# Kernel optimization log

Hardware: AMD Instinct MI355X
Metric: run time of the kernel (lower is better)

The kernel has to match this reference:

```python
import jax, jax.numpy as jnp
import numpy as np


def setup_inputs() -> dict:
    key = jax.random.key(0)
    ks = jax.random.split(key, 8)
    B, S, H = 16, 512, 1024
    K, E, L = 32, 1024, 2  # max_node_length, max_edge_length=K**2, num_labels
    seq = jax.random.normal(ks[0], (B, S, H), jnp.float32)
    # structured cumulative proof offsets: col0=1 ('<s>' offset, skipped by forward),
    # then n increasing offsets, zeros terminate. n <= K-1 so NAF node fits in K slots.
    rng = np.random.default_rng(0)
    off = np.zeros((B, K), np.int64)
    off[:, 0] = 1
    for b in range(B):
        n = int(rng.integers(8, K))  # 8..31 segment nodes
        lens = rng.integers(4, 14, size=n)
        off[b, 1:n + 1] = np.cumsum(lens)  # max < 31*13+1 < S
    s = 0.02
    w = lambda k, shp: jax.random.normal(k, shp, jnp.float32) * s
    return {
        'sequence_outputs': seq,
        'proof_offsets': jnp.asarray(off),
        'naf_W': w(ks[1], (H, H)), 'naf_b': jnp.zeros((H,), jnp.float32),
        'cls_dense_W': w(ks[2], (H, H)), 'cls_dense_b': jnp.zeros((H,), jnp.float32),
        'cls_out_W': w(ks[3], (H, L)), 'cls_out_b': jnp.zeros((L,), jnp.float32),
        'node_dense_W': w(ks[4], (H, H)), 'node_dense_b': jnp.zeros((H,), jnp.float32),
        'node_out_W': w(ks[5], (H, L)), 'node_out_b': jnp.zeros((L,), jnp.float32),
        'edge_dense_W': w(ks[6], (3 * H, H)), 'edge_dense_b': jnp.zeros((H,), jnp.float32),
        'edge_out_W': w(ks[7], (H, L)), 'edge_out_b': jnp.zeros((L,), jnp.float32),
        'max_node_length': K,
        'max_edge_length': E,
    }


def _head(x, dW, db, oW, ob):
    # dropout is identity in eval mode
    return jnp.tanh(x @ dW + db) @ oW + ob


def reference(sequence_outputs, proof_offsets,
              naf_W, naf_b, cls_dense_W, cls_dense_b, cls_out_W, cls_out_b,
              node_dense_W, node_dense_b, node_out_W, node_out_b,
              edge_dense_W, edge_dense_b, edge_out_W, edge_out_b,
              max_node_length, max_edge_length):
    B, S, H = sequence_outputs.shape
    K = max_node_length
    E = max_edge_length
    cls_tok = sequence_outputs[:, 0, :]                      # [B,H]
    naf = cls_tok @ naf_W + naf_b                            # [B,H]
    logits = _head(cls_tok, cls_dense_W, cls_dense_b, cls_out_W, cls_out_b)  # [B,L]

    # segment-mean pooling over variable-length spans
    off = proof_offsets[:, 1:]                               # [B,K-1] cumulative offsets
    valid = off > 0                                          # [B,K-1]
    n = valid.sum(axis=1)                                    # [B] #segment nodes
    starts = jnp.concatenate([jnp.ones((B, 1), off.dtype), off[:, :-1] + 1], axis=1)
    pos = jnp.arange(S)
    mask = ((pos[None, None, :] >= starts[:, :, None])
            & (pos[None, None, :] <= off[:, :, None])
            & valid[:, :, None]).astype(sequence_outputs.dtype)  # [B,K-1,S]
    sums = jnp.einsum('bks,bsh->bkh', mask, sequence_outputs)
    counts = mask.sum(axis=-1, keepdims=True)
    node_emb = sums / jnp.maximum(counts, 1.0)               # [B,K-1,H]

    # place segment nodes in slots [0,n), NAF at slot n, zeros after (padded batch buffer)
    slots = jnp.arange(K)
    is_naf = slots[None, :] == n[:, None]
    is_node = slots[None, :] < n[:, None]
    node_emb_p = jnp.pad(node_emb, ((0, 0), (0, 1), (0, 0)))  # [B,K,H]
    full_nodes = jnp.where(is_naf[:, :, None], naf[:, None, :],
                           jnp.where(is_node[:, :, None], node_emb_p, 0.0))  # [B,K,H]

    node_logits = _head(full_nodes, node_dense_W, node_dense_b, node_out_W, node_out_b)

    # pairwise edge features, row-major flattened per sample with m=n+1 nodes:
    # edge[i*m+j] = [node[j], node[i], node[j]-node[i]]
    m = n + 1                                                # [B]
    e = jnp.arange(E)
    i_idx = e[None, :] // m[:, None]                         # [B,E]
    j_idx = e[None, :] % m[:, None]
    valid_e = e[None, :] < (m * m)[:, None]
    i_c = jnp.clip(i_idx, 0, K - 1)
    j_c = jnp.clip(j_idx, 0, K - 1)
    ni = jnp.take_along_axis(full_nodes, i_c[:, :, None], axis=1)  # [B,E,H]
    nj = jnp.take_along_axis(full_nodes, j_c[:, :, None], axis=1)
    edge_feat = jnp.where(valid_e[:, :, None],
                          jnp.concatenate([nj, ni, nj - ni], axis=-1), 0.0)  # [B,E,3H]

    edge_logits = _head(edge_feat, edge_dense_W, edge_dense_b, edge_out_W, edge_out_b)

    return logits, node_logits, edge_logits
```

## Files before the change

### kernel.cpp

```cpp
#include <hip/hip_runtime.h>
#include <hip/hip_bf16.h>

typedef __hip_bfloat16 bf16;
typedef unsigned short ushort;
typedef __attribute__((ext_vector_type(8))) short short8v;
typedef __attribute__((ext_vector_type(4))) float float4v;

__device__ __forceinline__ float us2f(unsigned int u) {
    union { unsigned int i; float f; } c; c.i = u << 16; return c.f;
}
__device__ __forceinline__ bf16 f2bf(float x) { return __float2bfloat16(x); }
__device__ __forceinline__ ushort f2bfu(float x) {
    union { float f; unsigned int i; } c; c.f = x;
    unsigned int lsb = (c.i >> 16) & 1;
    return (ushort)((c.i + 0x7FFF + lsb) >> 16);
}
__device__ __forceinline__ float fcf(float x) {
    return fminf(1000.f, fmaxf(-1000.f, x));
}
__device__ __forceinline__ int iclamp(int v, int lo, int hi) {
    return v < lo ? lo : (v > hi ? hi : v);
}

__device__ __forceinline__ int po_ps(const int* po) {
    return ((po[1] | po[3] | po[5]) == 0) ? 2 : 1;
}
__device__ __forceinline__ int count_n(const int* po, int b, int ps) {
    int n = 0;
    #pragma unroll
    for (int j = 1; j < 32; ++j) n += (po[(b * 32 + j) * ps] > 0) ? 1 : 0;
    return iclamp(n, 0, 31);
}

__global__ __launch_bounds__(256) void k_sentinel(float* __restrict__ out, int nv, float val) {
    int i = blockIdx.x * 256 + threadIdx.x;
    if (i < nv) out[i] = val;
}


__device__ __forceinline__ void dev_prep(int kt, int nt, int z, int tid,
                                         const float* __restrict__ ndW,
                                         const float* __restrict__ eW,
                                         ushort* __restrict__ Wct, float* smemf)
{
    float (*T)[33] = (float (*)[33])smemf;

    const int k_loc = tid >> 3, n0 = (tid & 7) * 4;
    const size_t gofs = (size_t)(kt * 32 + k_loc) * 1024 + nt * 32 + n0;
    float4 v;
    if (z == 0) {
        v = *(const float4*)(ndW + gofs);
    } else if (z == 1) {
        float4 a = *(const float4*)(eW + gofs);
        float4 b = *(const float4*)(eW + (size_t)2048 * 1024 + gofs);
        v = make_float4(a.x + b.x, a.y + b.y, a.z + b.z, a.w + b.w);
    } else {
        float4 a = *(const float4*)(eW + (size_t)1024 * 1024 + gofs);
        float4 b = *(const float4*)(eW + (size_t)2048 * 1024 + gofs);
        v = make_float4(a.x - b.x, a.y - b.y, a.z - b.z, a.w - b.w);
    }
    T[k_loc][n0 + 0] = v.x; T[k_loc][n0 + 1] = v.y;
    T[k_loc][n0 + 2] = v.z; T[k_loc][n0 + 3] = v.w;
    __syncthreads();

    const int n_loc = tid >> 3, k0 = (tid & 7) * 4;
    ushort* dst = Wct + (size_t)z * 1024 * 1024 + (size_t)(nt * 32 + n_loc) * 1024 + kt * 32 + k0;
    ushort4 o;
    o.x = f2bfu(T[k0 + 0][n_loc]); o.y = f2bfu(T[k0 + 1][n_loc]);
    o.z = f2bfu(T[k0 + 2][n_loc]); o.w = f2bfu(T[k0 + 3][n_loc]);
    *(ushort4*)dst = o;
}

__device__ __forceinline__ void dev_nodes(int bx, int tid,
                                          const float* __restrict__ seq,
                                          const int* __restrict__ po,
                                          bf16* __restrict__ fn, int bbase)
{
    const int b_loc = bx >> 5;
    const int k = bx & 31;
    const int b = bbase + b_loc;
    const int ps = po_ps(po);
    const int n = count_n(po, b, ps);
    if (k == n) return;

    const int h0 = tid * 4;
    float4 acc = make_float4(0.f, 0.f, 0.f, 0.f);
    if (k < n) {
        int s_end   = iclamp(po[(b * 32 + k + 1) * ps], 1, 511);
        int s_begin = (k == 0) ? 1 : iclamp(po[(b * 32 + k) * ps] + 1, 1, 511);
        if (s_end < s_begin) s_end = s_begin;
        const float inv = 1.0f / (float)(s_end - s_begin + 1);
        for (int s = s_begin; s <= s_end; ++s) {
            float4 u = *(const float4*)(seq + ((size_t)(b * 512 + s)) * 1024 + h0);
            acc.x += u.x; acc.y += u.y; acc.z += u.z; acc.w += u.w;
        }
        acc.x *= inv; acc.y *= inv; acc.z *= inv; acc.w *= inv;
    }
    bf16* dst = fn + (size_t)(b_loc * 32 + k) * 1024 + h0;
    dst[0] = f2bf(acc.x); dst[1] = f2bf(acc.y); dst[2] = f2bf(acc.z); dst[3] = f2bf(acc.w);
}

__device__ __forceinline__ void dev_cls(int b_loc, int q, int tid,
                                        const float* __restrict__ seq,
                                        const int* __restrict__ po,
                                        const float* __restrict__ nafW, const float* __restrict__ nafb,
                                        const float* __restrict__ clsW, const float* __restrict__ clsb,
                                        const float* __restrict__ clsoW,
                                        bf16* __restrict__ fn,
                                        float* __restrict__ cacc,
                                        int bbase, float* smemf)
{
    const int b = bbase + b_loc;
    const int c = tid & 63, kq = tid >> 6;
    const int hout = q * 64 + c;
    float* xs  = smemf;
    float* red = smemf + 1024;
    for (int j = tid; j < 1024; j += 256) xs[j] = seq[(size_t)b * 524288 + j];
    __syncthreads();

    float ca = 0.f, na = 0.f;
    const int kb = kq * 256;
    for (int i = 0; i < 256; ++i) {
        const int k = kb + i;
        float x = xs[k];
        ca = fmaf(x, clsW[(size_t)k * 1024 + hout], ca);
        na = fmaf(x, nafW[(size_t)k * 1024 + hout], na);
    }
    red[kq * 64 + c] = ca; red[(4 + kq) * 64 + c] = na;
    __syncthreads();
    if (kq == 0) {
        ca = red[0 * 64 + c] + red[1 * 64 + c] + red[2 * 64 + c] + red[3 * 64 + c];
        na = red[4 * 64 + c] + red[5 * 64 + c] + red[6 * 64 + c] + red[7 * 64 + c];
        const int ps = po_ps(po);
        const int n = count_n(po, b, ps);
        fn[(size_t)(b_loc * 32 + n) * 1024 + hout] = f2bf(na + nafb[hout]);
        float h = tanhf(ca + clsb[hout]);
        float2 ow = ((const float2*)clsoW)[hout];
        float q0 = h * ow.x, q1 = h * ow.y;
        #pragma unroll
        for (int off = 32; off > 0; off >>= 1) {
            q0 += __shfl_down(q0, off, 64);
            q1 += __shfl_down(q1, off, 64);
        }
        if (c == 0) {
            cacc[(b_loc * 16 + q) * 2 + 0] = q0;
            cacc[(b_loc * 16 + q) * 2 + 1] = q1;
        }
    }
}

__device__ __forceinline__ void dev_econ(int tid,
                                         const float* __restrict__ edb,
                                         const float* __restrict__ eoW,
                                         float* __restrict__ econ)
{
    if (tid >= 64) return;
    const int lane = tid;
    float a0 = 0.f, a1 = 0.f;
    #pragma unroll
    for (int c = 0; c < 16; ++c) {
        const int idx = c * 64 + lane;
        float t = tanhf(edb[idx]);
        float2 ow = ((const float2*)eoW)[idx];
        a0 = fmaf(t, ow.x, a0);
        a1 = fmaf(t, ow.y, a1);
    }
    #pragma unroll
    for (int off = 32; off > 0; off >>= 1) {
        a0 += __shfl_down(a0, off, 64);
        a1 += __shfl_down(a1, off, 64);
    }
    if (lane == 0) { econ[0] = a0; econ[1] = a1; }
}

__global__ __launch_bounds__(256) void k_fusedA(const float* __restrict__ seq,
                                                const int* __restrict__ po,
                                                const float* __restrict__ nafW, const float* __restrict__ nafb,
                                                const float* __restrict__ clsW, const float* __restrict__ clsb,
                                                const float* __restrict__ clsoW,
                                                const float* __restrict__ ndW,
                                                const float* __restrict__ eW,
                                                const float* __restrict__ edb,
                                                const float* __restrict__ eoW,
                                                bf16* __restrict__ fn,
                                                float* __restrict__ cacc,
                                                ushort* __restrict__ Wct,
                                                float* __restrict__ econ)
{
    __shared__ float smem[1536];
    const int blk = blockIdx.x;
    const int tid = threadIdx.x;
    if (blk < 3072) {
        const int z = blk >> 10, rem = blk & 1023;
        dev_prep(rem & 31, rem >> 5, z, tid, ndW, eW, Wct, smem);
    } else if (blk < 3584) {
        dev_nodes(blk - 3072, tid, seq, po, fn, 0);
    } else if (blk < 3840) {
        const int r = blk - 3584;
        dev_cls(r & 15, r >> 4, tid, seq, po, nafW, nafb, clsW, clsb, clsoW, fn, cacc, 0, smem);
    } else {
        dev_econ(tid, edb, eoW, econ);
    }
}

__global__ __launch_bounds__(256) void k_nodes(const float* __restrict__ seq,
                                               const int* __restrict__ po,
                                               bf16* __restrict__ fn, int bbase)
{
    dev_nodes(blockIdx.x, threadIdx.x, seq, po, fn, bbase);
}
__global__ __launch_bounds__(256) void k_cls(const float* __restrict__ seq,
                                             const int* __restrict__ po,
                                             const float* __restrict__ nafW, const float* __restrict__ nafb,
                                             const float* __restrict__ clsW, const float* __restrict__ clsb,
                                             const float* __restrict__ clsoW,
                                             bf16* __restrict__ fn,
                                             float* __restrict__ cacc, int bbase)
{
    __shared__ float smem[1536];
    dev_cls(blockIdx.x, blockIdx.y, threadIdx.x, seq, po, nafW, nafb, clsW, clsb, clsoW, fn, cacc, bbase, smem);
}

__global__ __launch_bounds__(256) void k_huv_mfma(const bf16* __restrict__ X,
                                                  const ushort* __restrict__ Wct,
                                                  const float* __restrict__ ndb,
                                                  const float* __restrict__ noW,
                                                  float* __restrict__ nacc,
                                                  bf16* __restrict__ U,
                                                  bf16* __restrict__ V)
{
    const int rt = blockIdx.x;
    const int cc = blockIdx.y;
    const int z  = blockIdx.z;
    const int tid = threadIdx.x;
    const int w = tid >> 6, lane = tid & 63;
    const int quad = lane >> 4, l16 = lane & 15;
    const int rbase = rt * 16;

    __shared__ char smem[32768];
    short* A_lds = (short*)smem;
    float* Rs    = (float*)smem;

    {
        const int r = tid >> 4, s = tid & 15;
        const ushort* src = (const ushort*)X + (size_t)(rbase + r) * 1024 + s * 64;
        #pragma unroll
        for (int cch = 0; cch < 8; ++cch) {
            const int k0 = s * 64 + cch * 8;
            uint4 v = *(const uint4*)(src + cch * 8);
            const int slot = ((k0 >> 5) * 64 + ((k0 >> 3) & 3) * 16 + r) * 8;
            *(uint4*)&A_lds[slot] = v;
        }
    }
    __syncthreads();

    const ushort* Wz = Wct + (size_t)z * 1024 * 1024;
    const int nbase = cc * 128 + w * 32;
    const ushort* B0 = Wz + (size_t)(nbase + l16) * 1024 + quad * 8;
    const ushort* B1 = B0 + (size_t)16 * 1024;

    float4v acc0 = {0.f, 0.f, 0.f, 0.f};
    float4v acc1 = {0.f, 0.f, 0.f, 0.f};

    #pragma unroll 4
    for (int ks = 0; ks < 1024; ks += 32) {
        short8v a  = *(const short8v*)&A_lds[((ks >> 5) * 64 + quad * 16 + l16) * 8];
        short8v b0 = *(const short8v*)(B0 + ks);
        short8v b1 = *(const short8v*)(B1 + ks);
        acc0 = __builtin_amdgcn_mfma_f32_16x16x32_bf16(a, b0, acc0, 0, 0, 0);
        acc1 = __builtin_amdgcn_mfma_f32_16x16x32_bf16(a, b1, acc1, 0, 0, 0);
    }
    __syncthreads();

    #pragma unroll
    for (int reg = 0; reg < 4; ++reg) {
        Rs[(quad * 4 + reg) * 128 + w * 32 + l16]      = acc0[reg];
        Rs[(quad * 4 + reg) * 128 + w * 32 + 16 + l16] = acc1[reg];
    }
    __syncthreads();

    const int row = tid >> 4;
    const int c0 = (tid & 15) * 8;
    const int gcol0 = cc * 128 + c0;
    const float* src = &Rs[row * 128 + c0];
    float s[8];
    {
        float4 a = ((const float4*)src)[0];
        float4 b = ((const float4*)src)[1];
        s[0] = a.x; s[1] = a.y; s[2] = a.z; s[3] = a.w;
        s[4] = b.x; s[5] = b.y; s[6] = b.z; s[7] = b.w;
    }
    if (z == 0) {
        float q0 = 0.f, q1 = 0.f;
        #pragma unroll
        for (int e = 0; e < 8; ++e) {
            float t = tanhf(s[e] + ndb[gcol0 + e]);
            float2 ow = ((const float2*)noW)[gcol0 + e];
            q0 = fmaf(t, ow.x, q0);
            q1 = fmaf(t, ow.y, q1);
        }
        #pragma unroll
        for (int off = 8; off > 0; off >>= 1) {
            q0 += __shfl_down(q0, off, 16);
            q1 += __shfl_down(q1, off, 16);
        }
        if ((tid & 15) == 0) {
            float* np = nacc + ((size_t)(rbase + row) * 8 + cc) * 2;
            np[0] = q0; np[1] = q1;
        }
    } else {
        bf16* dstbuf = (z == 1) ? U : V;
        bf16* dst = dstbuf + (size_t)(rbase + row) * 1024 + gcol0;
        #pragma unroll
        for (int e = 0; e < 8; ++e) dst[e] = f2bf(s[e]);
    }
}

__global__ __launch_bounds__(256) void k_huv_valu(const bf16* __restrict__ X,
                                                  const float* __restrict__ ndW, const float* __restrict__ ndb,
                                                  const float* __restrict__ noW,
                                                  const float* __restrict__ eW,
                                                  float* __restrict__ nacc,
                                                  bf16* __restrict__ U,
                                                  bf16* __restrict__ V)
{
    const int rt = blockIdx.x, cc = blockIdx.y, z = blockIdx.z;
    const int tid = threadIdx.x;
    const int w = tid >> 6, lane = tid & 63;
    const int rg = lane >> 4, cg = lane & 15;
    const int rbase = rt * 16;
    const int colb = cc * 128 + cg * 8;

    __shared__ float LDSb[8192];
    float* Xs = LDSb;
    float* Rs = LDSb;

    const float* W0;
    const float* W1 = nullptr;
    float sgn = 1.f;
    if (z == 0)      { W0 = ndW; }
    else if (z == 1) { W0 = eW; W1 = eW + (size_t)2048 * 1024; }
    else             { W0 = eW + (size_t)1024 * 1024; W1 = eW + (size_t)2048 * 1024; sgn = -1.f; }

    float acc[32];
    #pragma unroll
    for (int i = 0; i < 32; ++i) acc[i] = 0.f;

    const int sr = tid & 15, sq0 = tid >> 4;
    const ushort* Xu = (const ushort*)X;

    for (int ks = 0; ks < 1024; ks += 256) {
        __syncthreads();
        #pragma unroll
        for (int it = 0; it < 4; ++it) {
            int qq = sq0 + it * 16;
            ushort4 xv = *(const ushort4*)(Xu + (size_t)(rbase + sr) * 1024 + ks + qq * 4);
            int kk = qq * 4;
            Xs[(kk + 0) * 16 + sr] = us2f(xv.x);
            Xs[(kk + 1) * 16 + sr] = us2f(xv.y);
            Xs[(kk + 2) * 16 + sr] = us2f(xv.z);
            Xs[(kk + 3) * 16 + sr] = us2f(xv.w);
        }
        __syncthreads();
        const int k0 = ks + w * 64;
        for (int kk = 0; kk < 64; ++kk) {
            float4 xv = *(const float4*)&Xs[(w * 64 + kk) * 16 + rg * 4];
            const float* wp0 = W0 + (size_t)(k0 + kk) * 1024 + colb;
            float4 wa = ((const float4*)wp0)[0];
            float4 wb = ((const float4*)wp0)[1];
            if (W1) {
                const float* wp1 = W1 + (size_t)(k0 + kk) * 1024 + colb;
                float4 va = ((const float4*)wp1)[0];
                float4 vb = ((const float4*)wp1)[1];
                wa.x = fmaf(sgn, va.x, wa.x); wa.y = fmaf(sgn, va.y, wa.y);
                wa.z = fmaf(sgn, va.z, wa.z); wa.w = fmaf(sgn, va.w, wa.w);
                wb.x = fmaf(sgn, vb.x, wb.x); wb.y = fmaf(sgn, vb.y, wb.y);
                wb.z = fmaf(sgn, vb.z, wb.z); wb.w = fmaf(sgn, vb.w, wb.w);
            }
            float xr[4] = {xv.x, xv.y, xv.z, xv.w};
            #pragma unroll
            for (int rr = 0; rr < 4; ++rr) {
                acc[rr*8+0] = fmaf(xr[rr], wa.x, acc[rr*8+0]);
                acc[rr*8+1] = fmaf(xr[rr], wa.y, acc[rr*8+1]);
                acc[rr*8+2] = fmaf(xr[rr], wa.z, acc[rr*8+2]);
                acc[rr*8+3] = fmaf(xr[rr], wa.w, acc[rr*8+3]);
                acc[rr*8+4] = fmaf(xr[rr], wb.x, acc[rr*8+4]);
                acc[rr*8+5] = fmaf(xr[rr], wb.y, acc[rr*8+5]);
                acc[rr*8+6] = fmaf(xr[rr], wb.z, acc[rr*8+6]);
                acc[rr*8+7] = fmaf(xr[rr], wb.w, acc[rr*8+7]);
            }
        }
    }
    __syncthreads();
    #pragma unroll
    for (int rr = 0; rr < 4; ++rr) {
        float* dst = &Rs[w * 2048 + (rg * 4 + rr) * 128 + cg * 8];
        *(float4*)(dst)     = make_float4(acc[rr*8+0], acc[rr*8+1], acc[rr*8+2], acc[rr*8+3]);
        *(float4*)(dst + 4) = make_float4(acc[rr*8+4], acc[rr*8+5], acc[rr*8+6], acc[rr*8+7]);
    }
    __syncthreads();
    const int row = tid >> 4;
    const int c0 = (tid & 15) * 8;
    float s[8];
    #pragma unroll
    for (int e = 0; e < 8; ++e) s[e] = 0.f;
    #pragma unroll
    for (int ww = 0; ww < 4; ++ww) {
        const float* src = &Rs[ww * 2048 + row * 128 + c0];
        float4 a = ((const float4*)src)[0];
        float4 b = ((const float4*)src)[1];
        s[0] += a.x; s[1] += a.y; s[2] += a.z; s[3] += a.w;
        s[4] += b.x; s[5] += b.y; s[6] += b.z; s[7] += b.w;
    }
    const int gcol0 = cc * 128 + c0;
    if (z == 0) {
        float q0 = 0.f, q1 = 0.f;
        #pragma unroll
        for (int e = 0; e < 8; ++e) {
            float t = tanhf(s[e] + ndb[gcol0 + e]);
            float2 ow = ((const float2*)noW)[gcol0 + e];
            q0 = fmaf(t, ow.x, q0);
            q1 = fmaf(t, ow.y, q1);
        }
        #pragma unroll
        for (int off = 8; off > 0; off >>= 1) {
            q0 += __shfl_down(q0, off, 16);
            q1 += __shfl_down(q1, off, 16);
        }
        if ((tid & 15) == 0) {
            float* np = nacc + ((size_t)(rbase + row) * 8 + cc) * 2;
            np[0] = q0; np[1] = q1;
        }
    } else {
        bf16* dstbuf = (z == 1) ? U : V;
        bf16* dst = dstbuf + (size_t)(rbase + row) * 1024 + gcol0;
        #pragma unroll
        for (int e = 0; e < 8; ++e) dst[e] = f2bf(s[e]);
    }
}

__global__ __launch_bounds__(256) void k_fin2(const float* __restrict__ nacc,
                                              const float* __restrict__ cacc,
                                              const float* __restrict__ nob,
                                              const float* __restrict__ clsob,
                                              float* __restrict__ out,
                                              int bbase, int nb)
{
    const int idx = blockIdx.x * 256 + threadIdx.x;
    const int R = nb * 32;
    if (idx < R) {
        const float4* p = (const float4*)(nacc + (size_t)idx * 16);
        float4 a = p[0], b4 = p[1], c4 = p[2], d4 = p[3];
        float s0 = a.x + a.z + b4.x + b4.z + c4.x + c4.z + d4.x + d4.z;
        float s1 = a.y + a.w + b4.y + b4.w + c4.y + c4.w + d4.y + d4.w;
        out[32 + bbase * 64 + idx * 2 + 0] = fcf(s0 + nob[0]);
        out[32 + bbase * 64 + idx * 2 + 1] = fcf(s1 + nob[1]);
    } else if (idx < R + nb * 2) {
        const int c = idx - R;
        const int b = c >> 1, l = c & 1;
        float s = 0.f;
        for (int q = 0; q < 16; ++q) s += cacc[(b * 16 + q) * 2 + l];
        out[(bbase + b) * 2 + l] = fcf(s + clsob[l]);
    }
}

__global__ __launch_bounds__(256) void k_edge(const bf16* __restrict__ U,
                                              const bf16* __restrict__ V,
                                              const float* __restrict__ edb,
                                              const float* __restrict__ eoW, const float* __restrict__ eob,
                                              const int* __restrict__ po,
                                              float* __restrict__ out,
                                              int bbase)
{
    const int blk = blockIdx.x;
    const int b_loc = blk >> 8;
    const int b = bbase + b_loc;
    const int tid = threadIdx.x;
    const int w = tid >> 6, lane = tid & 63;
    const int e = (blk & 255) * 4 + w;
    const int ps = po_ps(po);
    const int n = count_n(po, b, ps);
    const int m = n + 1;
    const bool valid = e < m * m;
    int i = 0, j = 0;
    if (valid) { i = e / m; j = e - i * m; }
    i = iclamp(i, 0, 31); j = iclamp(j, 0, 31);

    const ushort* urow = (const ushort*)U + (size_t)(b_loc * 32 + j) * 1024;
    const ushort* vrow = (const ushort*)V + (size_t)(b_loc * 32 + i) * 1024;

    float a0 = 0.f, a1 = 0.f;
    #pragma unroll
    for (int c = 0; c < 16; ++c) {
        const int idx = c * 64 + lane;
        float p = edb[idx];
        if (valid) p += us2f(urow[idx]) + us2f(vrow[idx]);
        float t = tanhf(p);
        float2 ow = ((const float2*)eoW)[idx];
        a0 = fmaf(t, ow.x, a0);
        a1 = fmaf(t, ow.y, a1);
    }
    #pragma unroll
    for (int off = 32; off > 0; off >>= 1) {
        a0 += __shfl_down(a0, off, 64);
        a1 += __shfl_down(a1, off, 64);
    }
    if (lane == 0) {
        const size_t o = 32 + 1024 + (size_t)(b * 1024 + e) * 2;
        out[o + 0] = fcf(a0 + eob[0]);
        out[o + 1] = fcf(a1 + eob[1]);
    }
}

__global__ __launch_bounds__(256) void k_fusedC(const bf16* __restrict__ U,
                                                const bf16* __restrict__ V,
                                                const float* __restrict__ nacc,
                                                const float* __restrict__ cacc,
                                                const float* __restrict__ nob,
                                                const float* __restrict__ clsob,
                                                const float* __restrict__ edb,
                                                const float* __restrict__ eoW,
                                                const float* __restrict__ eob,
                                                const float* __restrict__ econ,
                                                const int* __restrict__ po,
                                                float* __restrict__ out)
{
    const int blk = blockIdx.x;
    const int tid = threadIdx.x;

    if (blk >= 4096) {
        const int idx = (blk - 4096) * 256 + tid;
        if (idx < 512) {
            const float4* p = (const float4*)(nacc + (size_t)idx * 16);
            float4 a = p[0], b4 = p[1], c4 = p[2], d4 = p[3];
            float s0 = a.x + a.z + b4.x + b4.z + c4.x + c4.z + d4.x + d4.z;
            float s1 = a.y + a.w + b4.y + b4.w + c4.y + c4.w + d4.y + d4.w;
            out[32 + idx * 2 + 0] = fcf(s0 + nob[0]);
            out[32 + idx * 2 + 1] = fcf(s1 + nob[1]);
        } else if (idx < 544) {
            const int c = idx - 512;
            const int b = c >> 1, l = c & 1;
            float s = 0.f;
            for (int q = 0; q < 16; ++q) s += cacc[(b * 16 + q) * 2 + l];
            out[b * 2 + l] = fcf(s + clsob[l]);
        }
        return;
    }

    const int b = blk >> 8;
    const int w = tid >> 6, lane = tid & 63;
    const int e = (blk & 255) * 4 + w;
    const int ps = po_ps(po);
    const int n = count_n(po, b, ps);
    const int m = n + 1;
    const size_t o = 32 + 1024 + (size_t)(b * 1024 + e) * 2;

    if (e >= m * m) {
        if (lane == 0) {
            out[o + 0] = fcf(econ[0] + eob[0]);
            out[o + 1] = fcf(econ[1] + eob[1]);
        }
        return;
    }

    int i = e / m, j = e - i * m;
    i = iclamp(i, 0, 31); j = iclamp(j, 0, 31);
    const ushort* urow = (const ushort*)U + (size_t)(b * 32 + j) * 1024;
    const ushort* vrow = (const ushort*)V + (size_t)(b * 32 + i) * 1024;

    float a0 = 0.f, a1 = 0.f;
    #pragma unroll
    for (int c = 0; c < 16; ++c) {
        const int idx = c * 64 + lane;
        float p = edb[idx] + us2f(urow[idx]) + us2f(vrow[idx]);
        float t = tanhf(p);
        float2 ow = ((const float2*)eoW)[idx];
        a0 = fmaf(t, ow.x, a0);
        a1 = fmaf(t, ow.y, a1);
    }
    #pragma unroll
    for (int off = 32; off > 0; off >>= 1) {
        a0 += __shfl_down(a0, off, 64);
        a1 += __shfl_down(a1, off, 64);
    }
    if (lane == 0) {
        out[o + 0] = fcf(a0 + eob[0]);
        out[o + 1] = fcf(a1 + eob[1]);
    }
}

extern "C" void kernel_launch(void* const* d_in, const int* in_sizes, int n_in,
                              void* d_out, int out_size, void* d_ws, size_t ws_size,
                              hipStream_t stream) {
    (void)out_size;
    float* out = (float*)d_out;

    bool ok = (n_in >= 16)
        && in_sizes[0] == 8388608 && in_sizes[1] == 512
        && in_sizes[2] == 1048576 && in_sizes[3] == 1024
        && in_sizes[4] == 1048576 && in_sizes[5] == 1024
        && in_sizes[6] == 2048    && in_sizes[7] == 2
        && in_sizes[8] == 1048576 && in_sizes[9] == 1024
        && in_sizes[10] == 2048   && in_sizes[11] == 2
        && in_sizes[12] == 3145728 && in_sizes[13] == 1024
        && in_sizes[14] == 2048   && in_sizes[15] == 2;
    if (!ok) {
        hipLaunchKernelGGL(k_sentinel, dim3(133), dim3(256), 0, stream, out, 33824, 111.0f);
        return;
    }

    const float* seq   = (const float*)d_in[0];
    const int*   po    = (const int*)d_in[1];
    const float* nafW  = (const float*)d_in[2];
    const float* nafb  = (const float*)d_in[3];
    const float* clsW  = (const float*)d_in[4];
    const float* clsb  = (const float*)d_in[5];
    const float* clsoW = (const float*)d_in[6];
    const float* clsob = (const float*)d_in[7];
    const float* ndW   = (const float*)d_in[8];
    const float* ndb   = (const float*)d_in[9];
    const float* noW   = (const float*)d_in[10];
    const float* nob   = (const float*)d_in[11];
    const float* eW    = (const float*)d_in[12];
    const float* edb   = (const float*)d_in[13];
    const float* eoW   = (const float*)d_in[14];
    const float* eob   = (const float*)d_in[15];

    char* ws = (char*)d_ws;

    const size_t fnB   = (size_t)512 * 1024 * 2;
    const size_t naccB = (size_t)512 * 8 * 2 * sizeof(float);
    const size_t caccB = (size_t)16 * 16 * 2 * sizeof(float);
    const size_t econB = 64;
    const size_t wctB  = (size_t)3 * 1024 * 1024 * 2;
    const size_t needA = 3 * fnB + naccB + caccB + econB + wctB;
    const size_t needB = 3 * fnB + naccB + caccB;
    const size_t fnC   = (size_t)32 * 1024 * 2;
    const size_t needC = 3 * fnC + (size_t)32 * 8 * 2 * sizeof(float) + (size_t)16 * 2 * sizeof(float);

    if (ws_size >= needA) {
        bf16*   fn   = (bf16*)(ws);
        bf16*   U    = (bf16*)(ws + fnB);
        bf16*   V    = (bf16*)(ws + 2 * fnB);
        float*  nacc = (float*)(ws + 3 * fnB);
        float*  cacc = (float*)(ws + 3 * fnB + naccB);
        float*  econ = (float*)(ws + 3 * fnB + naccB + caccB);
        ushort* Wct  = (ushort*)(ws + 3 * fnB + naccB + caccB + econB);
        hipLaunchKernelGGL(k_fusedA, dim3(3841), dim3(256), 0, stream,
                           seq, po, nafW, nafb, clsW, clsb, clsoW, ndW, eW, edb, eoW,
                           fn, cacc, Wct, econ);
        hipLaunchKernelGGL(k_huv_mfma, dim3(32, 8, 3), dim3(256), 0, stream,
                           fn, Wct, ndb, noW, nacc, U, V);
        hipLaunchKernelGGL(k_fusedC, dim3(4099), dim3(256), 0, stream,
                           U, V, nacc, cacc, nob, clsob, edb, eoW, eob, econ, po, out);
    } else if (ws_size >= needB) {
        bf16*  fn   = (bf16*)(ws);
        bf16*  U    = (bf16*)(ws + fnB);
        bf16*  V    = (bf16*)(ws + 2 * fnB);
        float* nacc = (float*)(ws + 3 * fnB);
        float* cacc = (float*)(ws + 3 * fnB + naccB);
        hipLaunchKernelGGL(k_nodes, dim3(512), dim3(256), 0, stream, seq, po, fn, 0);
        hipLaunchKernelGGL(k_cls, dim3(16, 16), dim3(256), 0, stream,
                           seq, po, nafW, nafb, clsW, clsb, clsoW, fn, cacc, 0);
        hipLaunchKernelGGL(k_huv_valu, dim3(32, 8, 3), dim3(256), 0, stream,
                           fn, ndW, ndb, noW, eW, nacc, U, V);
        hipLaunchKernelGGL(k_fin2, dim3(3), dim3(256), 0, stream, nacc, cacc, nob, clsob, out, 0, 16);
        hipLaunchKernelGGL(k_edge, dim3(4096), dim3(256), 0, stream,
                           U, V, edb, eoW, eob, po, out, 0);
    } else if (ws_size >= needC) {
        bf16*  fn   = (bf16*)(ws);
        bf16*  U    = (bf16*)(ws + fnC);
        bf16*  V    = (bf16*)(ws + 2 * fnC);
        float* nacc = (float*)(ws + 3 * fnC);
        float* cacc = nacc + 32 * 8 * 2;
        for (int b = 0; b < 16; ++b) {
            hipLaunchKernelGGL(k_nodes, dim3(32), dim3(256), 0, stream, seq, po, fn, b);
            hipLaunchKernelGGL(k_cls, dim3(1, 16), dim3(256), 0, stream,
                               seq, po, nafW, nafb, clsW, clsb, clsoW, fn, cacc, b);
            hipLaunchKernelGGL(k_huv_valu, dim3(2, 8, 3), dim3(256), 0, stream,
                               fn, ndW, ndb, noW, eW, nacc, U, V);
            hipLaunchKernelGGL(k_fin2, dim3(1), dim3(256), 0, stream, nacc, cacc, nob, clsob, out, b, 1);
            hipLaunchKernelGGL(k_edge, dim3(256), dim3(256), 0, stream,
                               U, V, edb, eoW, eob, po, out, b);
        }
    } else {
        hipLaunchKernelGGL(k_sentinel, dim3(133), dim3(256), 0, stream, out, 33824, 222.0f);
    }
}
```

Before: 193.2 us.

## Vectorize cls GEMV loads, unroll node mean loop, reorder fused block dispatch

The cls/naf GEMV now has each thread load float4 weight columns over a 64-row K slice, where before it made scalar loads over 256 rows. The 16 partial sums are then reduced through a larger shared buffer. The segment-mean loop in dev_nodes is unrolled by two with separate accumulators to get more loads in flight. In the fused kernel, the long-latency cls and node blocks are moved to the front of the grid so they start first instead of trailing the prep blocks. The cost is doubled shared memory per block, which may lower occupancy for the prep blocks.

After: 179.8 us (median of 3 runs). -6.9%, faster.

```diff
diff --git a/kernel.cpp b/kernel.cpp
--- a/kernel.cpp
+++ b/kernel.cpp
@@ -90,11 +90,21 @@
         int s_begin = (k == 0) ? 1 : iclamp(po[(b * 32 + k) * ps] + 1, 1, 511);
         if (s_end < s_begin) s_end = s_begin;
         const float inv = 1.0f / (float)(s_end - s_begin + 1);
-        for (int s = s_begin; s <= s_end; ++s) {
-            float4 u = *(const float4*)(seq + ((size_t)(b * 512 + s)) * 1024 + h0);
+        float4 acc2 = make_float4(0.f, 0.f, 0.f, 0.f);
+        int s = s_begin;
+        const float* base = seq + (size_t)b * 524288 + h0;
+        for (; s + 1 <= s_end; s += 2) {
+            float4 u = *(const float4*)(base + (size_t)s * 1024);
+            float4 v = *(const float4*)(base + (size_t)(s + 1) * 1024);
+            acc.x += u.x;  acc.y += u.y;  acc.z += u.z;  acc.w += u.w;
+            acc2.x += v.x; acc2.y += v.y; acc2.z += v.z; acc2.w += v.w;
+        }
+        if (s <= s_end) {
+            float4 u = *(const float4*)(base + (size_t)s * 1024);
             acc.x += u.x; acc.y += u.y; acc.z += u.z; acc.w += u.w;
         }
-        acc.x *= inv; acc.y *= inv; acc.z *= inv; acc.w *= inv;
+        acc.x = (acc.x + acc2.x) * inv; acc.y = (acc.y + acc2.y) * inv;
+        acc.z = (acc.z + acc2.z) * inv; acc.w = (acc.w + acc2.w) * inv;
     }
     bf16* dst = fn + (size_t)(b_loc * 32 + k) * 1024 + h0;
     dst[0] = f2bf(acc.x); dst[1] = f2bf(acc.y); dst[2] = f2bf(acc.z); dst[3] = f2bf(acc.w);
@@ -111,30 +121,46 @@
                                         int bbase, float* smemf)
 {
     const int b = bbase + b_loc;
-    const int c = tid & 63, kq = tid >> 6;
-    const int hout = q * 64 + c;
-    float* xs  = smemf;
-    float* red = smemf + 1024;
+    float* xs   = smemf;
+    float* redc = smemf + 1024;
+    float* redn = smemf + 2048;
     for (int j = tid; j < 1024; j += 256) xs[j] = seq[(size_t)b * 524288 + j];
     __syncthreads();
 
-    float ca = 0.f, na = 0.f;
-    const int kb = kq * 256;
-    for (int i = 0; i < 256; ++i) {
-        const int k = kb + i;
-        float x = xs[k];
-        ca = fmaf(x, clsW[(size_t)k * 1024 + hout], ca);
-        na = fmaf(x, nafW[(size_t)k * 1024 + hout], na);
-    }
-    red[kq * 64 + c] = ca; red[(4 + kq) * 64 + c] = na;
+    const int c16 = tid & 15, kq = tid >> 4;
+    const int col0 = q * 64 + c16 * 4;
+    const int kb = kq * 64;
+    const float* wc_base = clsW + (size_t)kb * 1024 + col0;
+    const float* wn_base = nafW + (size_t)kb * 1024 + col0;
+    float4 ac = make_float4(0.f, 0.f, 0.f, 0.f);
+    float4 an = make_float4(0.f, 0.f, 0.f, 0.f);
+    #pragma unroll 4
+    for (int i = 0; i < 64; ++i) {
+        const float x = xs[kb + i];
+        float4 wc = *(const float4*)(wc_base + (size_t)i * 1024);
+        float4 wn = *(const float4*)(wn_base + (size_t)i * 1024);
+        ac.x = fmaf(x, wc.x, ac.x); ac.y = fmaf(x, wc.y, ac.y);
+        ac.z = fmaf(x, wc.z, ac.z); ac.w = fmaf(x, wc.w, ac.w);
+        an.x = fmaf(x, wn.x, an.x); an.y = fmaf(x, wn.y, an.y);
+        an.z = fmaf(x, wn.z, an.z); an.w = fmaf(x, wn.w, an.w);
+    }
+    *(float4*)&redc[kq * 64 + c16 * 4] = ac;
+    *(float4*)&redn[kq * 64 + c16 * 4] = an;
     __syncthreads();
-    if (kq == 0) {
-        ca = red[0 * 64 + c] + red[1 * 64 + c] + red[2 * 64 + c] + red[3 * 64 + c];
-        na = red[4 * 64 + c] + red[5 * 64 + c] + red[6 * 64 + c] + red[7 * 64 + c];
+
+    if (tid < 64) {
+        const int cl = tid;
+        float cs = 0.f, ns = 0.f;
+        #pragma unroll
+        for (int kk = 0; kk < 16; ++kk) {
+            cs += redc[kk * 64 + cl];
+            ns += redn[kk * 64 + cl];
+        }
+        const int hout = q * 64 + cl;
         const int ps = po_ps(po);
         const int n = count_n(po, b, ps);
-        fn[(size_t)(b_loc * 32 + n) * 1024 + hout] = f2bf(na + nafb[hout]);
-        float h = tanhf(ca + clsb[hout]);
+        fn[(size_t)(b_loc * 32 + n) * 1024 + hout] = f2bf(ns + nafb[hout]);
+        float h = tanhf(cs + clsb[hout]);
         float2 ow = ((const float2*)clsoW)[hout];
         float q0 = h * ow.x, q1 = h * ow.y;
         #pragma unroll
@@ -142,7 +168,7 @@
             q0 += __shfl_down(q0, off, 64);
             q1 += __shfl_down(q1, off, 64);
         }
-        if (c == 0) {
+        if (cl == 0) {
             cacc[(b_loc * 16 + q) * 2 + 0] = q0;
             cacc[(b_loc * 16 + q) * 2 + 1] = q1;
         }
@@ -187,17 +213,17 @@
                                                 ushort* __restrict__ Wct,
                                                 float* __restrict__ econ)
 {
-    __shared__ float smem[1536];
+    __shared__ __align__(16) float smem[3072];
     const int blk = blockIdx.x;
     const int tid = threadIdx.x;
-    if (blk < 3072) {
-        const int z = blk >> 10, rem = blk & 1023;
-        dev_prep(rem & 31, rem >> 5, z, tid, ndW, eW, Wct, smem);
-    } else if (blk < 3584) {
-        dev_nodes(blk - 3072, tid, seq, po, fn, 0);
+    if (blk < 256) {
+        dev_cls(blk & 15, blk >> 4, tid, seq, po, nafW, nafb, clsW, clsb, clsoW, fn, cacc, 0, smem);
+    } else if (blk < 768) {
+        dev_nodes(blk - 256, tid, seq, po, fn, 0);
     } else if (blk < 3840) {
-        const int r = blk - 3584;
-        dev_cls(r & 15, r >> 4, tid, seq, po, nafW, nafb, clsW, clsb, clsoW, fn, cacc, 0, smem);
+        const int rem = blk - 768;
+        const int z = rem >> 10, t10 = rem & 1023;
+        dev_prep(t10 & 31, t10 >> 5, z, tid, ndW, eW, Wct, smem);
     } else {
         dev_econ(tid, edb, eoW, econ);
     }
@@ -217,7 +243,7 @@
                                              bf16* __restrict__ fn,
                                              float* __restrict__ cacc, int bbase)
 {
-    __shared__ float smem[1536];
+    __shared__ __align__(16) float smem[3072];
     dev_cls(blockIdx.x, blockIdx.y, threadIdx.x, seq, po, nafW, nafb, clsW, clsb, clsoW, fn, cacc, bbase, smem);
 }
 
```
